# Performance work log

Measured on AMD Instinct MI355X. Metric: run time of the kernel, lower is better.

## Reference

```python
import jax, jax.numpy as jnp
import numpy as np

S = 7
BB = 2          # boxes per cell
C = 20          # classes
L_COORD = 5.0
L_NOOBJ = 0.5
L_OBJ = 1.0
L_CLASS = 1.0
BATCH = 8192


def setup_inputs() -> dict:
    key = jax.random.key(0)
    k1, k2, k3, k4 = jax.random.split(key, 4)
    pred = jax.random.normal(k1, (BATCH, S, S, BB * 5 + C), dtype=jnp.float32)
    cls = jax.random.uniform(k2, (BATCH, S, S, C), dtype=jnp.float32)
    # obj conf must be exactly 1.0 where an object exists (obj_mask test is ==1)
    conf = (jax.random.uniform(k3, (BATCH, S, S, 1)) < 0.3).astype(jnp.float32)
    box = jax.random.uniform(k4, (BATCH, S, S, 4), dtype=jnp.float32)  # cx,cy,w,h in [0,1)
    target = jnp.concatenate([cls, conf, box], axis=-1)
    return {"pred": pred, "target": target}


def _iou(a, b):
    # a: (..., BB, 4) cx,cy,w,h ; b: (..., 1, 4)  -> iou (..., BB)
    ax1, ay1 = a[..., 0] - a[..., 2] / 2, a[..., 1] - a[..., 3] / 2
    ax2, ay2 = a[..., 0] + a[..., 2] / 2, a[..., 1] + a[..., 3] / 2
    bx1, by1 = b[..., 0] - b[..., 2] / 2, b[..., 1] - b[..., 3] / 2
    bx2, by2 = b[..., 0] + b[..., 2] / 2, b[..., 1] + b[..., 3] / 2
    iw = jnp.clip(jnp.minimum(ax2, bx2) - jnp.maximum(ax1, bx1), 0.0)
    ih = jnp.clip(jnp.minimum(ay2, by2) - jnp.maximum(ay1, by1), 0.0)
    inter = iw * ih
    union = jnp.abs(a[..., 2] * a[..., 3]) + jnp.abs(b[..., 2] * b[..., 3]) - inter
    return inter / (union + 1e-6)


def reference(pred, target):
    # pred: (N,S,S,B*5+C), target: (N,S,S,5+C)
    objf = (target[..., C] == 1.0).astype(pred.dtype)        # (N,S,S)
    noobjf = 1.0 - objf
    pred_boxes = pred[..., C:].reshape(-1, S, S, BB, 5)       # (N,S,S,B,5) [conf,cx,cy,w,h]
    tb = target[..., C:]                                      # (N,S,S,5)

    ious = _iou(pred_boxes[..., 1:], tb[..., None, 1:])       # (N,S,S,B)
    best = jnp.argmax(ious, axis=-1)                          # responsible box index
    iou_best = jnp.max(ious, axis=-1)                         # (N,S,S)
    pb = jnp.take_along_axis(pred_boxes, best[..., None, None], axis=3)[..., 0, :]  # (N,S,S,5)

    center = jnp.sum((tb[..., 1:3] - pb[..., 1:3]) ** 2, axis=-1)
    # pred wh: pow(2).sqrt().sqrt() == sqrt(|wh|)
    wh = jnp.sum((jnp.sqrt(tb[..., 3:]) - jnp.sqrt(jnp.abs(pb[..., 3:]))) ** 2, axis=-1)
    conf_sq = (tb[..., 0] - pb[..., 0]) ** 2
    cls_sq = jnp.sum((pred[..., :C] - target[..., :C]) ** 2, axis=-1)

    loss = jnp.sum(
        objf * (L_COORD * (center + wh) + L_OBJ * conf_sq + L_CLASS * cls_sq)
        + noobjf * L_NOOBJ * conf_sq
    )
    avg_iou = jnp.sum(iou_best * objf) / jnp.maximum(jnp.sum(objf), 1.0)
    return loss, avg_iou
```

## Files before the change

### kernel.cpp

```cpp
#include <hip/hip_runtime.h>
#include <stdint.h>

#define S 7
#define BB 2
#define CLS 20
#define NCHUNK (8192 * S * S / 64)
#define CPB 64
#define THREADS 64
#define GRID 1280
#define PRED_F 30
#define TGT_F 25

#define ASYNC_CP16(gsrc, ldst)                                                  \
    __builtin_amdgcn_global_load_lds(                                           \
        (const __attribute__((address_space(1))) void*)(gsrc),                  \
        (__attribute__((address_space(3))) void*)(ldst), 16, 0, 0)

#define WAIT_VM15()  __builtin_amdgcn_s_waitcnt(0x0F7F)
#define WAIT_VM0()   __builtin_amdgcn_s_waitcnt(0x0F70)
#define WAIT_LGKM0() __builtin_amdgcn_s_waitcnt(0xC07F)

__device__ __forceinline__ float iou_fn(float ax, float ay, float aw, float ah,
                                        float bx, float by, float bw, float bh) {
    float ax1 = ax - aw * 0.5f, ay1 = ay - ah * 0.5f;
    float ax2 = ax + aw * 0.5f, ay2 = ay + ah * 0.5f;
    float bx1 = bx - bw * 0.5f, by1 = by - bh * 0.5f;
    float bx2 = bx + bw * 0.5f, by2 = by + bh * 0.5f;
    float iw = fmaxf(fminf(ax2, bx2) - fmaxf(ax1, bx1), 0.0f);
    float ih = fmaxf(fminf(ay2, by2) - fmaxf(ay1, by1), 0.0f);
    float inter = iw * ih;
    float uni = fabsf(aw * ah) + fabsf(bw * bh) - inter;
    return inter / (uni + 1e-6f);
}

__device__ __forceinline__ void prefetch_chunk(const float* __restrict__ pred,
                                               const float* __restrict__ tgt,
                                               int c, float* lpb, float* ltb, int t) {
    const float* gp = pred + (size_t)c * (CPB * PRED_F) + t * 4;
    #pragma unroll
    for (int i = 0; i < 7; ++i) ASYNC_CP16(gp + i * 256, lpb + i * 256);
    if (t < 32) ASYNC_CP16(gp + 7 * 256, lpb + 7 * 256);
    const float* gt = tgt + (size_t)c * (CPB * TGT_F) + t * 4;
    #pragma unroll
    for (int i = 0; i < 6; ++i) ASYNC_CP16(gt + i * 256, ltb + i * 256);
    if (t < 16) ASYNC_CP16(gt + 6 * 256, ltb + 6 * 256);
}

__global__ __launch_bounds__(THREADS) void yolo_main(const float* __restrict__ pred,
                                                     const float* __restrict__ tgt,
                                                     float4* __restrict__ part) {
    __shared__ float lp[2][CPB * PRED_F];
    __shared__ float lt[2][CPB * TGT_F];

    const int b = blockIdx.x;
    const int t = threadIdx.x;
    const int nch = (NCHUNK - b + GRID - 1) / GRID;

    prefetch_chunk(pred, tgt, b, lp[0], lt[0], t);
    if (nch > 1) prefetch_chunk(pred, tgt, b + GRID, lp[1], lt[1], t);

    float accL = 0.f, accI = 0.f, accO = 0.f;

    for (int k = 0; k < nch; ++k) {
        if (k + 1 < nch) WAIT_VM15();
        else             WAIT_VM0();

        const float* pp = lp[k & 1] + t * PRED_F;
        const float* tp = lt[k & 1] + t * TGT_F;

        float tconf = tp[CLS + 0];
        float tx = tp[CLS + 1], ty = tp[CLS + 2], tw = tp[CLS + 3], th = tp[CLS + 4];

        float iou0 = iou_fn(pp[CLS + 1], pp[CLS + 2], pp[CLS + 3], pp[CLS + 4], tx, ty, tw, th);
        float iou1 = iou_fn(pp[CLS + 6], pp[CLS + 7], pp[CLS + 8], pp[CLS + 9], tx, ty, tw, th);
        int sel = (iou1 > iou0) ? 1 : 0;
        float iou_best = fmaxf(iou0, iou1);

        const float* pb = pp + CLS + sel * 5;
        float dx = tx - pb[1], dy = ty - pb[2];
        float center = dx * dx + dy * dy;
        float dw = sqrtf(tw) - sqrtf(fabsf(pb[3]));
        float dh = sqrtf(th) - sqrtf(fabsf(pb[4]));
        float wh = dw * dw + dh * dh;
        float dc = tconf - pb[0];
        float conf_sq = dc * dc;

        float cls_sq = 0.0f;
        #pragma unroll
        for (int j = 0; j < CLS; ++j) {
            float d = pp[j] - tp[j];
            cls_sq += d * d;
        }

        float objf = (tconf == 1.0f) ? 1.0f : 0.0f;
        accL += objf * (5.0f * (center + wh) + conf_sq + cls_sq)
              + (1.0f - objf) * 0.5f * conf_sq;
        accI += objf * iou_best;
        accO += objf;

        int cnext = b + (k + 2) * GRID;
        if (cnext < NCHUNK) {
            WAIT_LGKM0();
            prefetch_chunk(pred, tgt, cnext, lp[k & 1], lt[k & 1], t);
        }
    }

    #pragma unroll
    for (int off = 32; off > 0; off >>= 1) {
        accL += __shfl_down(accL, off, 64);
        accI += __shfl_down(accI, off, 64);
        accO += __shfl_down(accO, off, 64);
    }
    if (t == 0) {
        part[b] = make_float4(accL, accI, accO, 0.0f);
    }
}

__global__ __launch_bounds__(256) void yolo_fin(const float4* __restrict__ part,
                                                float* __restrict__ out) {
    __shared__ float red[3][256 / 64];
    float l = 0.f, i = 0.f, o = 0.f;
    for (int k = threadIdx.x; k < GRID; k += 256) {
        float4 v = part[k];
        l += v.x;
        i += v.y;
        o += v.z;
    }
    #pragma unroll
    for (int off = 32; off > 0; off >>= 1) {
        l += __shfl_down(l, off, 64);
        i += __shfl_down(i, off, 64);
        o += __shfl_down(o, off, 64);
    }
    const int wave = threadIdx.x >> 6, lane = threadIdx.x & 63;
    if (lane == 0) {
        red[0][wave] = l;
        red[1][wave] = i;
        red[2][wave] = o;
    }
    __syncthreads();
    if (threadIdx.x == 0) {
        float L = 0.f, I = 0.f, O = 0.f;
        #pragma unroll
        for (int w = 0; w < 4; ++w) {
            L += red[0][w];
            I += red[1][w];
            O += red[2][w];
        }
        out[0] = L;
        out[1] = I / fmaxf(O, 1.0f);
    }
}

extern "C" void kernel_launch(void* const* d_in, const int* in_sizes, int n_in,
                              void* d_out, int out_size, void* d_ws, size_t ws_size,
                              hipStream_t stream) {
    const float* pred = (const float*)d_in[0];
    const float* tgt  = (const float*)d_in[1];
    float* out = (float*)d_out;
    float4* part = (float4*)d_ws;

    yolo_main<<<GRID, THREADS, 0, stream>>>(pred, tgt, part);
    yolo_fin<<<1, 256, 0, stream>>>(part, out);
}
```

Baseline: 107.4 us.

## Fuse final reduction into main kernel via flags, fix grid to four chunks per block

Merges the separate finalize kernel into the main kernel. Each block publishes its partial sums plus a release flag, and the last block spins on all flags to do the final reduction. This removes a second kernel launch and its dependency gap. The grid also changes to 1568 blocks, each handling exactly four chunks in a fully unrolled loop with no bounds checks. The flags are never reset between calls, so on later calls the last block can read stale partials before other blocks overwrite them. The spin-wait also assumes every block is eventually scheduled while the last block is waiting.

```diff
diff --git a/kernel.cpp b/kernel.cpp
--- a/kernel.cpp
+++ b/kernel.cpp
@@ -7,7 +7,8 @@
 #define NCHUNK (8192 * S * S / 64)
 #define CPB 64
 #define THREADS 64
-#define GRID 1280
+#define GRID 1568
+#define NCH 4
 #define PRED_F 30
 #define TGT_F 25
 
@@ -46,23 +47,27 @@
     if (t < 16) ASYNC_CP16(gt + 6 * 256, ltb + 6 * 256);
 }
 
-__global__ __launch_bounds__(THREADS) void yolo_main(const float* __restrict__ pred,
-                                                     const float* __restrict__ tgt,
-                                                     float4* __restrict__ part) {
+__global__ __launch_bounds__(THREADS) void yolo_fused(const float* __restrict__ pred,
+                                                      const float* __restrict__ tgt,
+                                                      float* __restrict__ pl,
+                                                      float* __restrict__ pi,
+                                                      float* __restrict__ po,
+                                                      uint32_t* __restrict__ flags,
+                                                      float* __restrict__ out) {
     __shared__ float lp[2][CPB * PRED_F];
     __shared__ float lt[2][CPB * TGT_F];
 
     const int b = blockIdx.x;
     const int t = threadIdx.x;
-    const int nch = (NCHUNK - b + GRID - 1) / GRID;
 
     prefetch_chunk(pred, tgt, b, lp[0], lt[0], t);
-    if (nch > 1) prefetch_chunk(pred, tgt, b + GRID, lp[1], lt[1], t);
+    prefetch_chunk(pred, tgt, b + GRID, lp[1], lt[1], t);
 
     float accL = 0.f, accI = 0.f, accO = 0.f;
 
-    for (int k = 0; k < nch; ++k) {
-        if (k + 1 < nch) WAIT_VM15();
+    #pragma unroll
+    for (int k = 0; k < NCH; ++k) {
+        if (k + 1 < NCH) WAIT_VM15();
         else             WAIT_VM0();
 
         const float* pp = lp[k & 1] + t * PRED_F;
@@ -98,10 +103,9 @@
         accI += objf * iou_best;
         accO += objf;
 
-        int cnext = b + (k + 2) * GRID;
-        if (cnext < NCHUNK) {
+        if (k + 2 < NCH) {
             WAIT_LGKM0();
-            prefetch_chunk(pred, tgt, cnext, lp[k & 1], lt[k & 1], t);
+            prefetch_chunk(pred, tgt, b + (k + 2) * GRID, lp[k & 1], lt[k & 1], t);
         }
     }
 
@@ -112,43 +116,33 @@
         accO += __shfl_down(accO, off, 64);
     }
     if (t == 0) {
-        part[b] = make_float4(accL, accI, accO, 0.0f);
+        pl[b] = accL;
+        pi[b] = accI;
+        po[b] = accO;
+        __hip_atomic_store(&flags[b], 1u, __ATOMIC_RELEASE, __HIP_MEMORY_SCOPE_AGENT);
     }
-}
 
-__global__ __launch_bounds__(256) void yolo_fin(const float4* __restrict__ part,
-                                                float* __restrict__ out) {
-    __shared__ float red[3][256 / 64];
-    float l = 0.f, i = 0.f, o = 0.f;
-    for (int k = threadIdx.x; k < GRID; k += 256) {
-        float4 v = part[k];
-        l += v.x;
-        i += v.y;
-        o += v.z;
-    }
-    #pragma unroll
-    for (int off = 32; off > 0; off >>= 1) {
-        l += __shfl_down(l, off, 64);
-        i += __shfl_down(i, off, 64);
-        o += __shfl_down(o, off, 64);
-    }
-    const int wave = threadIdx.x >> 6, lane = threadIdx.x & 63;
-    if (lane == 0) {
-        red[0][wave] = l;
-        red[1][wave] = i;
-        red[2][wave] = o;
-    }
-    __syncthreads();
-    if (threadIdx.x == 0) {
+    if (b == GRID - 1) {
         float L = 0.f, I = 0.f, O = 0.f;
+        for (int k = t; k < GRID; k += 64) {
+            while (__hip_atomic_load(&flags[k], __ATOMIC_ACQUIRE,
+                                     __HIP_MEMORY_SCOPE_AGENT) != 1u) {
+                __builtin_amdgcn_s_sleep(2);
+            }
+            L += __hip_atomic_load(&pl[k], __ATOMIC_RELAXED, __HIP_MEMORY_SCOPE_AGENT);
+            I += __hip_atomic_load(&pi[k], __ATOMIC_RELAXED, __HIP_MEMORY_SCOPE_AGENT);
+            O += __hip_atomic_load(&po[k], __ATOMIC_RELAXED, __HIP_MEMORY_SCOPE_AGENT);
+        }
         #pragma unroll
-        for (int w = 0; w < 4; ++w) {
-            L += red[0][w];
-            I += red[1][w];
-            O += red[2][w];
+        for (int off = 32; off > 0; off >>= 1) {
+            L += __shfl_down(L, off, 64);
+            I += __shfl_down(I, off, 64);
+            O += __shfl_down(O, off, 64);
         }
-        out[0] = L;
-        out[1] = I / fmaxf(O, 1.0f);
+        if (t == 0) {
+            out[0] = L;
+            out[1] = I / fmaxf(O, 1.0f);
+        }
     }
 }
 
@@ -158,8 +152,11 @@
     const float* pred = (const float*)d_in[0];
     const float* tgt  = (const float*)d_in[1];
     float* out = (float*)d_out;
-    float4* part = (float4*)d_ws;
 
-    yolo_main<<<GRID, THREADS, 0, stream>>>(pred, tgt, part);
-    yolo_fin<<<1, 256, 0, stream>>>(part, out);
+    float* pl = (float*)d_ws;
+    float* pi = pl + GRID;
+    float* po = pi + GRID;
+    uint32_t* flags = (uint32_t*)(po + GRID);
+
+    yolo_fused<<<GRID, THREADS, 0, stream>>>(pred, tgt, pl, pi, po, flags, out);
 }
```

Result: slower. 157.3 us (+46.5%).
